# Kernel optimization log

Measured on AMD Instinct MI355X. Metric: run time of the kernel, lower is better.

Reference implementation:

```python
import jax, jax.numpy as jnp
import numpy as np

DIM = 512
HEADS = 8
HEAD_DIM = DIM // HEADS
SCALE = HEAD_DIM ** -0.5
EPS = 1e-5


def setup_inputs() -> dict:
    key = jax.random.key(0)
    ks = jax.random.split(key, 6)
    B, N, C = 4, 2048, DIM
    x = jax.random.normal(ks[0], (B, N, C), dtype=jnp.float32)
    w_qkv = jax.random.normal(ks[1], (C, 3 * C), dtype=jnp.float32) * (C ** -0.5)
    w_proj = jax.random.normal(ks[2], (C, C), dtype=jnp.float32) * (C ** -0.5)
    b_proj = jax.random.normal(ks[3], (C,), dtype=jnp.float32) * 0.02
    gamma = jnp.ones((C,), dtype=jnp.float32)
    beta = jnp.zeros((C,), dtype=jnp.float32)
    return {"x": x, "w_qkv": w_qkv, "w_proj": w_proj, "b_proj": b_proj,
            "gamma": gamma, "beta": beta}


def reference(x, w_qkv, w_proj, b_proj, gamma, beta):
    B, N, C = x.shape
    # LayerNorm over channel dim
    mu = jnp.mean(x, axis=-1, keepdims=True)
    var = jnp.mean(jnp.square(x - mu), axis=-1, keepdims=True)
    xn = (x - mu) * jax.lax.rsqrt(var + EPS) * gamma + beta
    # QKV projection (fp32, no bias)
    qkv = xn @ w_qkv  # [B, N, 3C]
    qkv = qkv.reshape(B, N, 3, HEADS, HEAD_DIM)
    q = jnp.transpose(qkv[:, :, 0], (0, 2, 1, 3))  # [B, H, N, D]
    k = jnp.transpose(qkv[:, :, 1], (0, 2, 1, 3))
    v = jnp.transpose(qkv[:, :, 2], (0, 2, 1, 3))
    attn = jnp.einsum('bhnd,bhmd->bhnm', q, k) * SCALE
    attn = jax.nn.softmax(attn, axis=-1)
    out = jnp.einsum('bhnm,bhmd->bhnd', attn, v)  # [B, H, N, D]
    out = jnp.transpose(out, (0, 2, 1, 3)).reshape(B, N, C)
    out = out @ w_proj + b_proj
    return x + out
```

## Files before the change

kernel.cpp:

```cpp
#include <hip/hip_runtime.h>
#include <hip/hip_bf16.h>
#include <math.h>

typedef _Float16 f16;
typedef _Float16 half8 __attribute__((ext_vector_type(8)));
typedef _Float16 half4 __attribute__((ext_vector_type(4)));
typedef float f32x4 __attribute__((ext_vector_type(4)));
typedef unsigned int uint;
typedef unsigned int u32x4 __attribute__((ext_vector_type(4)));

#define DIMC 512
#define HEADS 8
#define HD 64
#define BB 4
#define NN 2048
#define MM (BB*NN)
#define NQKV (3*DIMC)
#define SCALE 0.125f
#define LOG2E 1.44269504f
#define EPSLN 1e-5f

__device__ __forceinline__ void g2l16(const void* g, void* l) {
    __builtin_amdgcn_global_load_lds(
        (const __attribute__((address_space(1))) unsigned int*)g,
        (__attribute__((address_space(3))) unsigned int*)l, 16, 0, 0);
}

__device__ __forceinline__ void ln_rows(const float* __restrict__ x,
                                        const float* __restrict__ gamma,
                                        const float* __restrict__ beta,
                                        f16* __restrict__ xn, int blk) {
    int w = threadIdx.x >> 6;
    int lane = threadIdx.x & 63;
    int row = blk * 4 + w;
    const float* xr = x + (size_t)row * DIMC;
    float4 v0 = ((const float4*)xr)[lane * 2];
    float4 v1 = ((const float4*)xr)[lane * 2 + 1];
    float s = v0.x + v0.y + v0.z + v0.w + v1.x + v1.y + v1.z + v1.w;
#pragma unroll
    for (int off = 1; off < 64; off <<= 1) s += __shfl_xor(s, off);
    float mu = s * (1.0f / DIMC);
    float d0 = v0.x - mu, d1 = v0.y - mu, d2 = v0.z - mu, d3 = v0.w - mu;
    float d4 = v1.x - mu, d5 = v1.y - mu, d6 = v1.z - mu, d7 = v1.w - mu;
    float s2 = d0*d0 + d1*d1 + d2*d2 + d3*d3 + d4*d4 + d5*d5 + d6*d6 + d7*d7;
#pragma unroll
    for (int off = 1; off < 64; off <<= 1) s2 += __shfl_xor(s2, off);
    float rstd = rsqrtf(s2 * (1.0f / DIMC) + EPSLN);
    float4 g0 = ((const float4*)gamma)[lane * 2];
    float4 g1 = ((const float4*)gamma)[lane * 2 + 1];
    float4 b0 = ((const float4*)beta)[lane * 2];
    float4 b1 = ((const float4*)beta)[lane * 2 + 1];
    half8 o;
    o[0] = (f16)(d0 * rstd * g0.x + b0.x);
    o[1] = (f16)(d1 * rstd * g0.y + b0.y);
    o[2] = (f16)(d2 * rstd * g0.z + b0.z);
    o[3] = (f16)(d3 * rstd * g0.w + b0.w);
    o[4] = (f16)(d4 * rstd * g1.x + b1.x);
    o[5] = (f16)(d5 * rstd * g1.y + b1.y);
    o[6] = (f16)(d6 * rstd * g1.z + b1.z);
    o[7] = (f16)(d7 * rstd * g1.w + b1.w);
    ((half8*)(xn + (size_t)row * DIMC))[lane] = o;
}

__device__ __forceinline__ void transp_tile(const float* __restrict__ src,
                                            f16* __restrict__ dst,
                                            int R, int C, int k0, int n0) {
    __shared__ f16 t[32][72];
    int tid = threadIdx.x;
    int rr = tid >> 6, col = tid & 63;
#pragma unroll
    for (int p = 0; p < 8; p++) {
        int r = p * 4 + rr;
        t[r][col] = (f16)src[(size_t)(k0 + r) * C + n0 + col];
    }
    __syncthreads();
    int nl = tid >> 2, kc = (tid & 3) * 8;
    half8 v;
#pragma unroll
    for (int j = 0; j < 8; j++) v[j] = t[kc + j][nl];
    *(half8*)&dst[(size_t)(n0 + nl) * R + k0 + kc] = v;
}

__global__ __launch_bounds__(256) void prep_kernel(const float* __restrict__ x,
                                                   const float* __restrict__ gamma,
                                                   const float* __restrict__ beta,
                                                   const float* __restrict__ wqkv,
                                                   const float* __restrict__ wproj,
                                                   f16* __restrict__ xn,
                                                   f16* __restrict__ wqkvt,
                                                   f16* __restrict__ wprojt) {
    int bid = blockIdx.x;
    if (bid < 2048) {
        ln_rows(x, gamma, beta, xn, bid);
    } else if (bid < 2048 + 384) {
        int b2 = bid - 2048;
        int bx = b2 % 24, by = b2 / 24;
        transp_tile(wqkv, wqkvt, DIMC, NQKV, by * 32, bx * 64);
    } else {
        int b2 = bid - 2048 - 384;
        int bx = b2 % 8, by = b2 / 8;
        transp_tile(wproj, wprojt, DIMC, DIMC, by * 32, bx * 64);
    }
}

__device__ __forceinline__ void gemm128_loop(const char* Ag, const char* Bg,
                                             f16* As, f16* Bs, f32x4 (&acc)[4][4]) {
    int tid = threadIdx.x;
    int w = tid >> 6, lane = tid & 63, l15 = lane & 15, quad = lane >> 4;
    int wy = w >> 1, wx = w & 1;
    int off0 = w * 1024 + lane * 16;
#define QSTAGE(kk, b) do { \
    _Pragma("unroll") \
    for (int c = 0; c < 2; ++c) { \
        int off = c * 4096 + off0; \
        int row = off >> 6, col = off & 63; \
        g2l16(Ag + (size_t)row * 1024 + (kk) * 64 + col, (char*)As + (b) * 8192 + c * 4096 + w * 1024); \
        g2l16(Bg + (size_t)row * 1024 + (kk) * 64 + col, (char*)Bs + (b) * 8192 + c * 4096 + w * 1024); \
    } } while (0)
    QSTAGE(0, 0);
    __syncthreads();
    for (int kk = 0; kk < 16; ++kk) {
        int cb = kk & 1;
        if (kk < 15) QSTAGE(kk + 1, cb ^ 1);
        half8 af[4], bf[4];
#pragma unroll
        for (int i = 0; i < 4; ++i) {
            af[i] = *(const half8*)((const char*)As + cb * 8192 + ((wy * 64 + i * 16 + l15) << 6) + quad * 16);
            bf[i] = *(const half8*)((const char*)Bs + cb * 8192 + ((wx * 64 + i * 16 + l15) << 6) + quad * 16);
        }
#pragma unroll
        for (int i = 0; i < 4; ++i)
#pragma unroll
            for (int j = 0; j < 4; ++j)
                acc[i][j] = __builtin_amdgcn_mfma_f32_16x16x32_f16(af[i], bf[j], acc[i][j], 0, 0, 0);
        __syncthreads();
    }
#undef QSTAGE
}

__global__ __launch_bounds__(256) void gemm_qkv(const f16* __restrict__ xn,
                                                const f16* __restrict__ wt,
                                                f16* __restrict__ qb,
                                                f16* __restrict__ kbuf,
                                                f16* __restrict__ vtb) {
    __shared__ __align__(16) f16 As[2 * 128 * 32];
    __shared__ __align__(16) f16 Bs[2 * 128 * 32];
    int tid = threadIdx.x;
    int w = tid >> 6, lane = tid & 63, l15 = lane & 15, quad = lane >> 4;
    int wy = w >> 1, wx = w & 1;
    int m0 = blockIdx.y * 128, c0 = blockIdx.x * 128;
    f32x4 acc[4][4] = {};
    gemm128_loop((const char*)(xn + (size_t)m0 * DIMC),
                 (const char*)(wt + (size_t)c0 * DIMC), As, Bs, acc);
    int bx = blockIdx.x;
    if (bx < 8) {
        const float QS = SCALE * LOG2E;
        f16* dst = (bx < 4) ? qb : kbuf;
        float mul = (bx < 4) ? QS : 1.0f;
        int cb = (bx < 4) ? c0 : c0 - DIMC;
#pragma unroll
        for (int i = 0; i < 4; ++i)
#pragma unroll
            for (int j = 0; j < 4; ++j)
#pragma unroll
                for (int r = 0; r < 4; ++r) {
                    int m = m0 + wy * 64 + i * 16 + quad * 4 + r;
                    int c = cb + wx * 64 + j * 16 + l15;
                    int b = m >> 11, n = m & 2047;
                    int h = c >> 6, d = c & 63;
                    dst[(((size_t)(b * HEADS + h)) * NN + n) * HD + d] = (f16)(acc[i][j][r] * mul);
                }
    } else {
        __syncthreads();
        f16* T = (f16*)As + w * 512;
        int cb = c0 - 2 * DIMC;
        int dl = lane >> 2, mp = lane & 3;
#pragma unroll
        for (int i = 0; i < 4; ++i)
#pragma unroll
            for (int j = 0; j < 4; ++j) {
                half4 hv;
#pragma unroll
                for (int r = 0; r < 4; ++r) hv[r] = (f16)acc[i][j][r];
                *(half4*)&T[l15 * 20 + quad * 4] = hv;
                half4 rv = *(half4*)&T[dl * 20 + mp * 4];
                int c = cb + wx * 64 + j * 16 + dl;
                int m = m0 + wy * 64 + i * 16 + mp * 4;
                int b = m >> 11, n = m & 2047;
                int h = c >> 6, d = c & 63;
                *(half4*)&vtb[(((size_t)(b * HEADS + h)) * HD + d) * NN + n] = rv;
            }
    }
}

__global__ __launch_bounds__(256, 4) void attn_kernel(const f16* __restrict__ qb,
                                                      const f16* __restrict__ kbuf,
                                                      const f16* __restrict__ vtb,
                                                      f16* __restrict__ ao) {
    __shared__ __align__(16) f16 KV[8192];
    char* Kc = (char*)KV;
    char* Vc = (char*)(KV + 4096);
    int id = blockIdx.x;
    int xcd = id & 7, slot = id >> 3;
    int bh = xcd * 4 + (slot >> 4);
    int qt4 = slot & 15;
    int n0 = qt4 * 128;
    int tid = threadIdx.x, w = tid >> 6, lane = tid & 63, l15 = lane & 15, quad = lane >> 4;
    const f16* Kbase = kbuf + (size_t)bh * NN * HD;
    const f16* Vbase = vtb + (size_t)bh * HD * NN;
    const f16* Qbase = qb + (size_t)bh * NN * HD;
    half8 qf[2][2];
#pragma unroll
    for (int qt = 0; qt < 2; ++qt) {
        const f16* qr = Qbase + (size_t)(n0 + w * 32 + qt * 16 + l15) * HD + quad * 8;
        qf[qt][0] = *(const half8*)qr;
        qf[qt][1] = *(const half8*)(qr + 32);
    }
    f32x4 ot[2][4] = {};
    f32x4 lacc[2] = {};
    half8 ones8;
#pragma unroll
    for (int j = 0; j < 8; ++j) ones8[j] = (f16)1.0f;
    int srow = tid >> 2, part = (tid & 3) * 16;
    int sb = srow * 128, sx = (srow & 7) << 4;
    int scol = part * 2;
    int rx = (l15 & 7) << 4;
    half8 kp0, kp1, vp0, vp1;
    {
        const f16* kg = Kbase + (size_t)srow * HD + part;
        kp0 = ((const half8*)kg)[0]; kp1 = ((const half8*)kg)[1];
        const f16* vg = Vbase + (size_t)srow * NN + part;
        vp0 = ((const half8*)vg)[0]; vp1 = ((const half8*)vg)[1];
    }
    for (int it = 0; it < NN / 64; ++it) {
        __syncthreads();
        *(half8*)(Kc + sb + (scol ^ sx)) = kp0;
        *(half8*)(Kc + sb + ((scol + 16) ^ sx)) = kp1;
        *(half8*)(Vc + sb + (scol ^ sx)) = vp0;
        *(half8*)(Vc + sb + ((scol + 16) ^ sx)) = vp1;
        __syncthreads();
        if (it < NN / 64 - 1) {
            int kt0 = (it + 1) * 64;
            const f16* kg = Kbase + (size_t)(kt0 + srow) * HD + part;
            kp0 = ((const half8*)kg)[0]; kp1 = ((const half8*)kg)[1];
            const f16* vg = Vbase + (size_t)srow * NN + kt0 + part;
            vp0 = ((const half8*)vg)[0]; vp1 = ((const half8*)vg)[1];
        }
        f32x4 s0[4], s1[4];
        __builtin_amdgcn_s_setprio(1);
#pragma unroll
        for (int kt = 0; kt < 4; ++kt) {
            int rb = (kt * 16 + l15) * 128;
            half8 a0 = *(const half8*)(Kc + rb + ((quad * 16) ^ rx));
            half8 a1 = *(const half8*)(Kc + rb + ((64 + quad * 16) ^ rx));
            f32x4 z0 = {};
            z0 = __builtin_amdgcn_mfma_f32_16x16x32_f16(a0, qf[0][0], z0, 0, 0, 0);
            z0 = __builtin_amdgcn_mfma_f32_16x16x32_f16(a1, qf[0][1], z0, 0, 0, 0);
            s0[kt] = z0;
            f32x4 z1 = {};
            z1 = __builtin_amdgcn_mfma_f32_16x16x32_f16(a0, qf[1][0], z1, 0, 0, 0);
            z1 = __builtin_amdgcn_mfma_f32_16x16x32_f16(a1, qf[1][1], z1, 0, 0, 0);
            s1[kt] = z1;
        }
        __builtin_amdgcn_s_setprio(0);
        uint up[2][4][2];
#pragma unroll
        for (int kt = 0; kt < 4; ++kt) {
            up[0][kt][0] = __builtin_bit_cast(uint, __builtin_amdgcn_cvt_pkrtz(
                __builtin_amdgcn_exp2f(s0[kt][0]), __builtin_amdgcn_exp2f(s0[kt][1])));
            up[0][kt][1] = __builtin_bit_cast(uint, __builtin_amdgcn_cvt_pkrtz(
                __builtin_amdgcn_exp2f(s0[kt][2]), __builtin_amdgcn_exp2f(s0[kt][3])));
            up[1][kt][0] = __builtin_bit_cast(uint, __builtin_amdgcn_cvt_pkrtz(
                __builtin_amdgcn_exp2f(s1[kt][0]), __builtin_amdgcn_exp2f(s1[kt][1])));
            up[1][kt][1] = __builtin_bit_cast(uint, __builtin_amdgcn_cvt_pkrtz(
                __builtin_amdgcn_exp2f(s1[kt][2]), __builtin_amdgcn_exp2f(s1[kt][3])));
        }
        __builtin_amdgcn_s_setprio(1);
#pragma unroll
        for (int kc = 0; kc < 2; ++kc) {
            int cb = (kc * 64 + quad * 16) ^ rx;
            half8 av[4];
#pragma unroll
            for (int dt = 0; dt < 4; ++dt)
                av[dt] = *(const half8*)(Vc + (dt * 16 + l15) * 128 + cb);
#pragma unroll
            for (int qt = 0; qt < 2; ++qt) {
                u32x4 pw;
#pragma unroll
                for (int i = 0; i < 2; ++i) {
                    uint x = up[qt][kc * 2][i], y = up[qt][kc * 2 + 1][i];
                    asm volatile("v_permlane32_swap_b32 %0, %1" : "+v"(x), "+v"(y));
                    asm volatile("v_permlane16_swap_b32 %0, %1" : "+v"(x), "+v"(y));
                    pw[i] = x; pw[2 + i] = y;
                }
                half8 pb8 = __builtin_bit_cast(half8, pw);
                lacc[qt] = __builtin_amdgcn_mfma_f32_16x16x32_f16(ones8, pb8, lacc[qt], 0, 0, 0);
#pragma unroll
                for (int dt = 0; dt < 4; ++dt)
                    ot[qt][dt] = __builtin_amdgcn_mfma_f32_16x16x32_f16(av[dt], pb8, ot[qt][dt], 0, 0, 0);
            }
        }
        __builtin_amdgcn_s_setprio(0);
    }
    float inv[2] = { 1.0f / lacc[0][0], 1.0f / lacc[1][0] };
    __syncthreads();
    char* Tc = (char*)(KV + w * 2048);
#pragma unroll
    for (int qt = 0; qt < 2; ++qt)
#pragma unroll
        for (int dt = 0; dt < 4; ++dt) {
            half4 hv;
#pragma unroll
            for (int r = 0; r < 4; ++r) hv[r] = (f16)(ot[qt][dt][r] * inv[qt]);
            *(half4*)(Tc + (qt * 16 + l15) * 128 + ((dt * 32 + quad * 8) ^ rx)) = hv;
        }
    __syncthreads();
    int b = bh >> 3, h = bh & 7;
#pragma unroll
    for (int j = 0; j < 4; ++j) {
        int nl = j * 8 + (lane >> 3);
        int d16 = (lane & 7) * 16;
        half8 v = *(const half8*)(Tc + nl * 128 + (d16 ^ ((nl & 7) << 4)));
        int n = n0 + w * 32 + nl;
        *(half8*)&ao[((size_t)(b * NN + n)) * DIMC + h * HD + (lane & 7) * 8] = v;
    }
}

__global__ __launch_bounds__(256) void gemm_proj(const f16* __restrict__ aob,
                                                 const f16* __restrict__ wt,
                                                 const float* __restrict__ x,
                                                 const float* __restrict__ bias,
                                                 float* __restrict__ out) {
    __shared__ __align__(16) f16 As[2 * 128 * 32];
    __shared__ __align__(16) f16 Bs[2 * 64 * 32];
    int tid = threadIdx.x;
    int w = tid >> 6, lane = tid & 63, l15 = lane & 15, quad = lane >> 4;
    int m0 = blockIdx.y * 128, c0 = blockIdx.x * 64;
    const char* Ag = (const char*)(aob + (size_t)m0 * DIMC);
    const char* Bg = (const char*)(wt + (size_t)c0 * DIMC);
    f32x4 acc[2][4] = {};
    int off0 = w * 1024 + lane * 16;
#define PSTAGE(kk, b) do { \
    _Pragma("unroll") \
    for (int c = 0; c < 2; ++c) { \
        int off = c * 4096 + off0; \
        int row = off >> 6, col = off & 63; \
        g2l16(Ag + (size_t)row * 1024 + (kk) * 64 + col, (char*)As + (b) * 8192 + c * 4096 + w * 1024); \
    } \
    { \
        int off = tid * 16; \
        int row = off >> 6, col = off & 63; \
        g2l16(Bg + (size_t)row * 1024 + (kk) * 64 + col, (char*)Bs + (b) * 4096 + w * 1024); \
    } } while (0)
    PSTAGE(0, 0);
    __syncthreads();
    for (int kk = 0; kk < 16; ++kk) {
        int cb = kk & 1;
        if (kk < 15) PSTAGE(kk + 1, cb ^ 1);
        half8 af[2], bf[4];
#pragma unroll
        for (int i = 0; i < 2; ++i)
            af[i] = *(const half8*)((const char*)As + cb * 8192 + ((w * 32 + i * 16 + l15) << 6) + quad * 16);
#pragma unroll
        for (int j = 0; j < 4; ++j)
            bf[j] = *(const half8*)((const char*)Bs + cb * 4096 + ((j * 16 + l15) << 6) + quad * 16);
#pragma unroll
        for (int i = 0; i < 2; ++i)
#pragma unroll
            for (int j = 0; j < 4; ++j)
                acc[i][j] = __builtin_amdgcn_mfma_f32_16x16x32_f16(af[i], bf[j], acc[i][j], 0, 0, 0);
        __syncthreads();
    }
#undef PSTAGE
#pragma unroll
    for (int i = 0; i < 2; ++i)
#pragma unroll
        for (int j = 0; j < 4; ++j)
#pragma unroll
            for (int r = 0; r < 4; ++r) {
                int m = m0 + w * 32 + i * 16 + quad * 4 + r;
                int c = c0 + j * 16 + l15;
                out[(size_t)m * DIMC + c] = x[(size_t)m * DIMC + c] + bias[c] + acc[i][j][r];
            }
}

extern "C" void kernel_launch(void* const* d_in, const int* in_sizes, int n_in,
                              void* d_out, int out_size, void* d_ws, size_t ws_size,
                              hipStream_t stream) {
    (void)in_sizes; (void)n_in; (void)out_size; (void)ws_size;
    const float* x     = (const float*)d_in[0];
    const float* wqkv  = (const float*)d_in[1];
    const float* wproj = (const float*)d_in[2];
    const float* bproj = (const float*)d_in[3];
    const float* gamma = (const float*)d_in[4];
    const float* beta  = (const float*)d_in[5];
    float* out = (float*)d_out;

    char* ws = (char*)d_ws;
    f16* xn     = (f16*)ws;                 ws += (size_t)MM * DIMC * 2;
    f16* wqkvt  = (f16*)ws;                 ws += (size_t)NQKV * DIMC * 2;
    f16* wprojt = (f16*)ws;                 ws += (size_t)DIMC * DIMC * 2;
    f16* qbuf   = (f16*)ws;                 ws += (size_t)MM * DIMC * 2;
    f16* kbuf   = (f16*)ws;                 ws += (size_t)MM * DIMC * 2;
    f16* vtbuf  = (f16*)ws;                 ws += (size_t)MM * DIMC * 2;
    f16* aobuf  = (f16*)ws;                 ws += (size_t)MM * DIMC * 2;

    prep_kernel<<<2048 + 384 + 128, 256, 0, stream>>>(x, gamma, beta, wqkv, wproj,
                                                      xn, wqkvt, wprojt);
    gemm_qkv<<<dim3(NQKV / 128, MM / 128), 256, 0, stream>>>(xn, wqkvt, qbuf, kbuf, vtbuf);
    attn_kernel<<<NN / 128 * BB * HEADS, 256, 0, stream>>>(qbuf, kbuf, vtbuf, aobuf);
    gemm_proj<<<dim3(DIMC / 64, MM / 128), 256, 0, stream>>>(aobuf, wprojt, x, bproj, out);
}
```

Measured before the change: 157.4 us.

## Double-buffer K/V tiles in LDS using direct global-to-LDS loads

Replaces the register-staged K/V prefetch (global load into registers, then LDS store between two barriers) with global_load_lds async copies into a double-buffered 32KB LDS region. The next tile is issued into the alternate buffer while the current one is consumed, leaving one barrier per iteration. This drops the VGPR staging and the LDS write instructions. In exchange LDS use per block doubles, which may limit occupancy against the declared 4 blocks per CU. Correctness relies on the trailing barrier also waiting for the async loads to complete.

After: 157.0 us. About the same (-0.3%).

```diff
diff --git a/kernel.cpp b/kernel.cpp
--- a/kernel.cpp
+++ b/kernel.cpp
@@ -197,9 +197,7 @@
                                                       const f16* __restrict__ kbuf,
                                                       const f16* __restrict__ vtb,
                                                       f16* __restrict__ ao) {
-    __shared__ __align__(16) f16 KV[8192];
-    char* Kc = (char*)KV;
-    char* Vc = (char*)(KV + 4096);
+    __shared__ __align__(16) f16 KV[16384];
     int id = blockIdx.x;
     int xcd = id & 7, slot = id >> 3;
     int bh = xcd * 4 + (slot >> 4);
@@ -221,30 +219,39 @@
     half8 ones8;
 #pragma unroll
     for (int j = 0; j < 8; ++j) ones8[j] = (f16)1.0f;
-    int srow = tid >> 2, part = (tid & 3) * 16;
-    int sb = srow * 128, sx = (srow & 7) << 4;
-    int scol = part * 2;
     int rx = (l15 & 7) << 4;
-    half8 kp0, kp1, vp0, vp1;
+    int lrow = lane >> 3;
+    int scolb = ((lane & 7) << 4) ^ (lrow << 4);
+    int rbase = w * 16;
     {
-        const f16* kg = Kbase + (size_t)srow * HD + part;
-        kp0 = ((const half8*)kg)[0]; kp1 = ((const half8*)kg)[1];
-        const f16* vg = Vbase + (size_t)srow * NN + part;
-        vp0 = ((const half8*)vg)[0]; vp1 = ((const half8*)vg)[1];
-    }
+        char* K0 = (char*)KV;
+        char* V0 = (char*)KV + 8192;
+#pragma unroll
+        for (int c = 0; c < 2; ++c) {
+            int r0 = rbase + c * 8;
+            g2l16((const char*)Kbase + (size_t)(r0 + lrow) * (HD * 2) + scolb,
+                  K0 + r0 * 128);
+            g2l16((const char*)Vbase + (size_t)(r0 + lrow) * (NN * 2) + scolb,
+                  V0 + r0 * 128);
+        }
+    }
+    __syncthreads();
     for (int it = 0; it < NN / 64; ++it) {
-        __syncthreads();
-        *(half8*)(Kc + sb + (scol ^ sx)) = kp0;
-        *(half8*)(Kc + sb + ((scol + 16) ^ sx)) = kp1;
-        *(half8*)(Vc + sb + (scol ^ sx)) = vp0;
-        *(half8*)(Vc + sb + ((scol + 16) ^ sx)) = vp1;
-        __syncthreads();
+        int cur = it & 1;
+        char* Kc = (char*)KV + (cur << 14);
+        char* Vc = Kc + 8192;
         if (it < NN / 64 - 1) {
-            int kt0 = (it + 1) * 64;
-            const f16* kg = Kbase + (size_t)(kt0 + srow) * HD + part;
-            kp0 = ((const half8*)kg)[0]; kp1 = ((const half8*)kg)[1];
-            const f16* vg = Vbase + (size_t)srow * NN + kt0 + part;
-            vp0 = ((const half8*)vg)[0]; vp1 = ((const half8*)vg)[1];
+            char* Kn = (char*)KV + ((cur ^ 1) << 14);
+            char* Vn = Kn + 8192;
+            int k0 = (it + 1) * 64;
+#pragma unroll
+            for (int c = 0; c < 2; ++c) {
+                int r0 = rbase + c * 8;
+                g2l16((const char*)Kbase + (size_t)(k0 + r0 + lrow) * (HD * 2) + scolb,
+                      Kn + r0 * 128);
+                g2l16((const char*)Vbase + (size_t)(r0 + lrow) * (NN * 2) + k0 * 2 + scolb,
+                      Vn + r0 * 128);
+            }
         }
         f32x4 s0[4], s1[4];
         __builtin_amdgcn_s_setprio(1);
@@ -301,10 +308,10 @@
             }
         }
         __builtin_amdgcn_s_setprio(0);
+        __syncthreads();
     }
     float inv[2] = { 1.0f / lacc[0][0], 1.0f / lacc[1][0] };
-    __syncthreads();
-    char* Tc = (char*)(KV + w * 2048);
+    char* Tc = (char*)KV + w * 4096;
 #pragma unroll
     for (int qt = 0; qt < 2; ++qt)
 #pragma unroll
```
